# Kernel tuning notes

Measured on AMD Instinct MI355X. Metric: run time of the kernel, lower is better.

## Reference

```python
import jax, jax.numpy as jnp
import numpy as np

N, M, D = 4096, 8192, 512

def setup_inputs() -> dict:
    key = jax.random.key(0)
    k1, k2, k3, k4 = jax.random.split(key, 4)
    X = jax.random.normal(k1, (N, D), dtype=jnp.float32)
    SV = jax.random.normal(k2, (M, D), dtype=jnp.float32)
    DC = jax.random.normal(k3, (1, M), dtype=jnp.float32)
    IC = jax.random.normal(k4, (1,), dtype=jnp.float32)
    gamma = jnp.float32(1.0 / D)
    return {"X": X, "SV": SV, "DC": DC, "IC": IC, "gamma": gamma}

def reference(X, SV, DC, IC, gamma):
    # Squared pairwise L2 distances via GEMM expansion (same math as
    # ||SV - x||^2 without materializing the [N, M, D] broadcast tensor):
    # d2[n, m] = ||x_n||^2 + ||sv_m||^2 - 2 * x_n . sv_m
    x2 = jnp.sum(X * X, axis=1)          # [N]
    sv2 = jnp.sum(SV * SV, axis=1)       # [M]
    cross = jnp.einsum("nd,md->nm", X, SV)  # [N, M]
    d2 = jnp.maximum(x2[:, None] + sv2[None, :] - 2.0 * cross, 0.0)
    k = jnp.exp(-gamma * d2)             # RBF kernel values [N, M]
    # Weighted reduction over support vectors + intercept -> decision values [N]
    return jnp.sum(k * DC, axis=1) + IC
```

## Files before the change

### kernel.cpp

```cpp
#include <hip/hip_runtime.h>
#include <stdint.h>

#define NN 4096
#define MM 8192
#define DD 512
#define KT 8

typedef __bf16 bf16x8 __attribute__((ext_vector_type(8)));
typedef __bf16 bf16x4 __attribute__((ext_vector_type(4)));
typedef float f32x4 __attribute__((ext_vector_type(4)));
typedef float f32x16 __attribute__((ext_vector_type(16)));

__device__ __forceinline__ void load_lds16(const void* g, void* l) {
  __builtin_amdgcn_global_load_lds(
      (const __attribute__((address_space(1))) unsigned int*)g,
      (__attribute__((address_space(3))) unsigned int*)l, 16, 0, 0);
}

__global__ __launch_bounds__(256) void convert_norm_kernel(
    const float* __restrict__ X, const float* __restrict__ SV,
    __bf16* __restrict__ Xb, __bf16* __restrict__ SVb,
    float* __restrict__ x2, float* __restrict__ sv2,
    float* __restrict__ out, const float* __restrict__ IC) {
  int wid = blockIdx.x * 4 + (threadIdx.x >> 6);
  int lane = threadIdx.x & 63;
  const float* src;
  __bf16* dst;
  float* nrm;
  if (wid < NN) {
    src = X + (size_t)wid * DD;
    dst = Xb + (size_t)wid * DD;
    nrm = x2 + wid;
    if (lane == 0) out[wid] = IC[0];
  } else {
    int r = wid - NN;
    src = SV + (size_t)r * DD;
    dst = SVb + (size_t)r * DD;
    nrm = sv2 + r;
  }
  const f32x4* s = (const f32x4*)src;
  f32x4 a = s[lane];
  f32x4 b = s[lane + 64];
  float sum = a.x * a.x + a.y * a.y + a.z * a.z + a.w * a.w +
              b.x * b.x + b.y * b.y + b.z * b.z + b.w * b.w;
  bf16x4 ca = {(__bf16)a.x, (__bf16)a.y, (__bf16)a.z, (__bf16)a.w};
  bf16x4 cb = {(__bf16)b.x, (__bf16)b.y, (__bf16)b.z, (__bf16)b.w};
  *(bf16x4*)(dst + 4 * lane) = ca;
  *(bf16x4*)(dst + 256 + 4 * lane) = cb;
#pragma unroll
  for (int m = 32; m >= 1; m >>= 1) sum += __shfl_xor(sum, m, 64);
  if (lane == 0) *nrm = sum;
}

__global__ __launch_bounds__(384, 3) void rbf_gemm_kernel(
    const bf16x8* __restrict__ Xb, const bf16x8* __restrict__ SVb,
    const float* __restrict__ x2, const float* __restrict__ sv2,
    const float* __restrict__ DC, const float* __restrict__ gamma_p,
    float* __restrict__ out) {
  __shared__ bf16x8 As[2][1024];
  __shared__ bf16x8 Bs[2][1024];

  const int t = threadIdx.x;
  const int lane = t & 63;
  const int wave = t >> 6;
  const int n0 = blockIdx.x * 128;
  const int m0 = blockIdx.y * 128;

  const int wave_m = wave & 1;
  const int wave_n = wave >> 1;
  const int l31 = lane & 31;
  const int lhi = lane >> 5;

  const int rg = lane >> 3;
  const int perm = (lane & 7) ^ rg;

  f32x16 acc[2][2];
#pragma unroll
  for (int i = 0; i < 2; ++i)
#pragma unroll
    for (int j = 0; j < 2; ++j)
#pragma unroll
      for (int r = 0; r < 16; ++r) acc[i][j][r] = 0.0f;

  if (wave == 4) {
#pragma unroll
    for (int it = 0; it < 16; ++it)
      load_lds16(Xb + (size_t)(n0 + it * 8 + rg) * 64 + perm, &As[0][it * 64 + lane]);
  } else if (wave == 5) {
#pragma unroll
    for (int it = 0; it < 16; ++it)
      load_lds16(SVb + (size_t)(m0 + it * 8 + rg) * 64 + perm, &Bs[0][it * 64 + lane]);
  }
  __syncthreads();

#pragma unroll
  for (int kt = 0; kt < KT; ++kt) {
    const int cur = kt & 1;
    const int nxt = cur ^ 1;
    if (wave == 4) {
      if (kt + 1 < KT) {
#pragma unroll
        for (int it = 0; it < 16; ++it)
          load_lds16(Xb + (size_t)(n0 + it * 8 + rg) * 64 + (kt + 1) * 8 + perm,
                     &As[nxt][it * 64 + lane]);
      }
    } else if (wave == 5) {
      if (kt + 1 < KT) {
#pragma unroll
        for (int it = 0; it < 16; ++it)
          load_lds16(SVb + (size_t)(m0 + it * 8 + rg) * 64 + (kt + 1) * 8 + perm,
                     &Bs[nxt][it * 64 + lane]);
      }
    } else {
#pragma unroll
      for (int ks = 0; ks < 4; ++ks) {
        const int kc = ks * 2 + lhi;
        const int sw = kc ^ (l31 & 7);
        const int ra = (wave_n * 64 + l31) * 8;
        const int rb = (wave_m * 64 + l31) * 8;
        bf16x8 af0 = As[cur][ra + sw];
        bf16x8 af1 = As[cur][ra + 256 + sw];
        bf16x8 bf0 = Bs[cur][rb + sw];
        bf16x8 bf1 = Bs[cur][rb + 256 + sw];
        acc[0][0] = __builtin_amdgcn_mfma_f32_32x32x16_bf16(af0, bf0, acc[0][0], 0, 0, 0);
        acc[0][1] = __builtin_amdgcn_mfma_f32_32x32x16_bf16(af0, bf1, acc[0][1], 0, 0, 0);
        acc[1][0] = __builtin_amdgcn_mfma_f32_32x32x16_bf16(af1, bf0, acc[1][0], 0, 0, 0);
        acc[1][1] = __builtin_amdgcn_mfma_f32_32x32x16_bf16(af1, bf1, acc[1][1], 0, 0, 0);
      }
    }
    __syncthreads();
  }

  if (wave < 4) {
    const float g = gamma_p[0];
    const float c2 = g * 1.4426950408889634f;

    float sv2v[2], dcv[2];
    const int colb = m0 + wave_m * 64 + l31;
    sv2v[0] = sv2[colb];
    dcv[0] = DC[colb];
    sv2v[1] = sv2[colb + 32];
    dcv[1] = DC[colb + 32];

#pragma unroll
    for (int i = 0; i < 2; ++i) {
      const int rowb = n0 + wave_n * 64 + i * 32 + 4 * lhi;
      float val[16];
#pragma unroll
      for (int g4 = 0; g4 < 4; ++g4) {
        f32x4 xv = *(const f32x4*)(x2 + rowb + 8 * g4);
#pragma unroll
        for (int r2 = 0; r2 < 4; ++r2) {
          const int reg = g4 * 4 + r2;
          float v = 0.0f;
#pragma unroll
          for (int j = 0; j < 2; ++j) {
            float d2 = xv[r2] + sv2v[j] - 2.0f * acc[i][j][reg];
            d2 = fmaxf(d2, 0.0f);
            v += exp2f(-c2 * d2) * dcv[j];
          }
          val[reg] = v;
        }
      }
#pragma unroll
      for (int m = 1; m < 32; m <<= 1)
#pragma unroll
        for (int reg = 0; reg < 16; ++reg)
          val[reg] += __shfl_xor(val[reg], m, 64);
      if (l31 == 0) {
#pragma unroll
        for (int g4 = 0; g4 < 4; ++g4)
#pragma unroll
          for (int r2 = 0; r2 < 4; ++r2)
            atomicAdd(&out[rowb + 8 * g4 + r2], val[g4 * 4 + r2]);
      }
    }
  }
}

extern "C" void kernel_launch(void* const* d_in, const int* in_sizes, int n_in,
                              void* d_out, int out_size, void* d_ws, size_t ws_size,
                              hipStream_t stream) {
  const float* X = (const float*)d_in[0];
  const float* SV = (const float*)d_in[1];
  const float* DC = (const float*)d_in[2];
  const float* IC = (const float*)d_in[3];
  const float* gamma = (const float*)d_in[4];
  float* out = (float*)d_out;

  char* ws = (char*)d_ws;
  __bf16* Xb = (__bf16*)ws;
  __bf16* SVb = (__bf16*)(ws + (size_t)NN * DD * 2);
  float* x2 = (float*)(ws + (size_t)(NN + MM) * DD * 2);
  float* sv2 = x2 + NN;

  convert_norm_kernel<<<(NN + MM) / 4, 256, 0, stream>>>(X, SV, Xb, SVb, x2, sv2, out, IC);
  dim3 grid(NN / 128, MM / 128);
  rbf_gemm_kernel<<<grid, 384, 0, stream>>>((const bf16x8*)Xb, (const bf16x8*)SVb,
                                            x2, sv2, DC, gamma, out);
}
```

Baseline: 151.2 us.

## Replace producer-wave double buffering with single-buffer cooperative loads

Drops the two dedicated loader waves and the double-buffered LDS. All four compute waves now cooperatively load each K tile into a single buffer, synchronize, then run the MFMAs. This halves LDS use and removes the idle producer waves, so more blocks can fit per CU (launch bounds raised to 4). The cost is that global-to-LDS loads are no longer overlapped with compute inside a block, and the design relies on other resident blocks to hide that latency.

After: 136.7 us. 9.6% less time.

```diff
diff --git a/kernel.cpp b/kernel.cpp
--- a/kernel.cpp
+++ b/kernel.cpp
@@ -52,13 +52,13 @@
   if (lane == 0) *nrm = sum;
 }
 
-__global__ __launch_bounds__(384, 3) void rbf_gemm_kernel(
+__global__ __launch_bounds__(256, 4) void rbf_gemm_kernel(
     const bf16x8* __restrict__ Xb, const bf16x8* __restrict__ SVb,
     const float* __restrict__ x2, const float* __restrict__ sv2,
     const float* __restrict__ DC, const float* __restrict__ gamma_p,
     float* __restrict__ out) {
-  __shared__ bf16x8 As[2][1024];
-  __shared__ bf16x8 Bs[2][1024];
+  __shared__ bf16x8 As[1024];
+  __shared__ bf16x8 Bs[1024];
 
   const int t = threadIdx.x;
   const int lane = t & 63;
@@ -71,8 +71,8 @@
   const int l31 = lane & 31;
   const int lhi = lane >> 5;
 
-  const int rg = lane >> 3;
-  const int perm = (lane & 7) ^ rg;
+  const int srow = t >> 3;
+  const int sslot = t & 7;
 
   f32x16 acc[2][2];
 #pragma unroll
@@ -82,98 +82,75 @@
 #pragma unroll
       for (int r = 0; r < 16; ++r) acc[i][j][r] = 0.0f;
 
-  if (wave == 4) {
+  for (int kt = 0; kt < KT; ++kt) {
 #pragma unroll
-    for (int it = 0; it < 16; ++it)
-      load_lds16(Xb + (size_t)(n0 + it * 8 + rg) * 64 + perm, &As[0][it * 64 + lane]);
-  } else if (wave == 5) {
+    for (int it = 0; it < 4; ++it) {
+      const int c = it * 256 + t;
+      const int row = it * 32 + srow;
+      const int kg = sslot ^ (row & 7);
+      load_lds16(Xb + (size_t)(n0 + row) * 64 + kt * 8 + kg, &As[c]);
+      load_lds16(SVb + (size_t)(m0 + row) * 64 + kt * 8 + kg, &Bs[c]);
+    }
+    __syncthreads();
 #pragma unroll
-    for (int it = 0; it < 16; ++it)
-      load_lds16(SVb + (size_t)(m0 + it * 8 + rg) * 64 + perm, &Bs[0][it * 64 + lane]);
-  }
-  __syncthreads();
-
-#pragma unroll
-  for (int kt = 0; kt < KT; ++kt) {
-    const int cur = kt & 1;
-    const int nxt = cur ^ 1;
-    if (wave == 4) {
-      if (kt + 1 < KT) {
-#pragma unroll
-        for (int it = 0; it < 16; ++it)
-          load_lds16(Xb + (size_t)(n0 + it * 8 + rg) * 64 + (kt + 1) * 8 + perm,
-                     &As[nxt][it * 64 + lane]);
-      }
-    } else if (wave == 5) {
-      if (kt + 1 < KT) {
-#pragma unroll
-        for (int it = 0; it < 16; ++it)
-          load_lds16(SVb + (size_t)(m0 + it * 8 + rg) * 64 + (kt + 1) * 8 + perm,
-                     &Bs[nxt][it * 64 + lane]);
-      }
-    } else {
-#pragma unroll
-      for (int ks = 0; ks < 4; ++ks) {
-        const int kc = ks * 2 + lhi;
-        const int sw = kc ^ (l31 & 7);
-        const int ra = (wave_n * 64 + l31) * 8;
-        const int rb = (wave_m * 64 + l31) * 8;
-        bf16x8 af0 = As[cur][ra + sw];
-        bf16x8 af1 = As[cur][ra + 256 + sw];
-        bf16x8 bf0 = Bs[cur][rb + sw];
-        bf16x8 bf1 = Bs[cur][rb + 256 + sw];
-        acc[0][0] = __builtin_amdgcn_mfma_f32_32x32x16_bf16(af0, bf0, acc[0][0], 0, 0, 0);
-        acc[0][1] = __builtin_amdgcn_mfma_f32_32x32x16_bf16(af0, bf1, acc[0][1], 0, 0, 0);
-        acc[1][0] = __builtin_amdgcn_mfma_f32_32x32x16_bf16(af1, bf0, acc[1][0], 0, 0, 0);
-        acc[1][1] = __builtin_amdgcn_mfma_f32_32x32x16_bf16(af1, bf1, acc[1][1], 0, 0, 0);
-      }
+    for (int ks = 0; ks < 4; ++ks) {
+      const int kc = ks * 2 + lhi;
+      const int sw = kc ^ (l31 & 7);
+      const int ra = (wave_n * 64 + l31) * 8;
+      const int rb = (wave_m * 64 + l31) * 8;
+      bf16x8 af0 = As[ra + sw];
+      bf16x8 af1 = As[ra + 256 + sw];
+      bf16x8 bf0 = Bs[rb + sw];
+      bf16x8 bf1 = Bs[rb + 256 + sw];
+      acc[0][0] = __builtin_amdgcn_mfma_f32_32x32x16_bf16(af0, bf0, acc[0][0], 0, 0, 0);
+      acc[0][1] = __builtin_amdgcn_mfma_f32_32x32x16_bf16(af0, bf1, acc[0][1], 0, 0, 0);
+      acc[1][0] = __builtin_amdgcn_mfma_f32_32x32x16_bf16(af1, bf0, acc[1][0], 0, 0, 0);
+      acc[1][1] = __builtin_amdgcn_mfma_f32_32x32x16_bf16(af1, bf1, acc[1][1], 0, 0, 0);
     }
     __syncthreads();
   }
 
-  if (wave < 4) {
-    const float g = gamma_p[0];
-    const float c2 = g * 1.4426950408889634f;
+  const float g = gamma_p[0];
+  const float c2 = g * 1.4426950408889634f;
 
-    float sv2v[2], dcv[2];
-    const int colb = m0 + wave_m * 64 + l31;
-    sv2v[0] = sv2[colb];
-    dcv[0] = DC[colb];
-    sv2v[1] = sv2[colb + 32];
-    dcv[1] = DC[colb + 32];
+  float sv2v[2], dcv[2];
+  const int colb = m0 + wave_m * 64 + l31;
+  sv2v[0] = sv2[colb];
+  dcv[0] = DC[colb];
+  sv2v[1] = sv2[colb + 32];
+  dcv[1] = DC[colb + 32];
 
 #pragma unroll
-    for (int i = 0; i < 2; ++i) {
-      const int rowb = n0 + wave_n * 64 + i * 32 + 4 * lhi;
-      float val[16];
+  for (int i = 0; i < 2; ++i) {
+    const int rowb = n0 + wave_n * 64 + i * 32 + 4 * lhi;
+    float val[16];
 #pragma unroll
-      for (int g4 = 0; g4 < 4; ++g4) {
-        f32x4 xv = *(const f32x4*)(x2 + rowb + 8 * g4);
+    for (int g4 = 0; g4 < 4; ++g4) {
+      f32x4 xv = *(const f32x4*)(x2 + rowb + 8 * g4);
 #pragma unroll
-        for (int r2 = 0; r2 < 4; ++r2) {
-          const int reg = g4 * 4 + r2;
-          float v = 0.0f;
+      for (int r2 = 0; r2 < 4; ++r2) {
+        const int reg = g4 * 4 + r2;
+        float v = 0.0f;
 #pragma unroll
-          for (int j = 0; j < 2; ++j) {
-            float d2 = xv[r2] + sv2v[j] - 2.0f * acc[i][j][reg];
-            d2 = fmaxf(d2, 0.0f);
-            v += exp2f(-c2 * d2) * dcv[j];
-          }
-          val[reg] = v;
+        for (int j = 0; j < 2; ++j) {
+          float d2 = xv[r2] + sv2v[j] - 2.0f * acc[i][j][reg];
+          d2 = fmaxf(d2, 0.0f);
+          v += exp2f(-c2 * d2) * dcv[j];
         }
+        val[reg] = v;
       }
+    }
 #pragma unroll
-      for (int m = 1; m < 32; m <<= 1)
+    for (int m = 1; m < 32; m <<= 1)
 #pragma unroll
-        for (int reg = 0; reg < 16; ++reg)
-          val[reg] += __shfl_xor(val[reg], m, 64);
-      if (l31 == 0) {
+      for (int reg = 0; reg < 16; ++reg)
+        val[reg] += __shfl_xor(val[reg], m, 64);
+    if (l31 == 0) {
 #pragma unroll
-        for (int g4 = 0; g4 < 4; ++g4)
+      for (int g4 = 0; g4 < 4; ++g4)
 #pragma unroll
-          for (int r2 = 0; r2 < 4; ++r2)
-            atomicAdd(&out[rowb + 8 * g4 + r2], val[g4 * 4 + r2]);
-      }
+        for (int r2 = 0; r2 < 4; ++r2)
+          atomicAdd(&out[rowb + 8 * g4 + r2], val[g4 * 4 + r2]);
     }
   }
 }
@@ -196,6 +173,6 @@
 
   convert_norm_kernel<<<(NN + MM) / 4, 256, 0, stream>>>(X, SV, Xb, SVb, x2, sv2, out, IC);
   dim3 grid(NN / 128, MM / 128);
-  rbf_gemm_kernel<<<grid, 384, 0, stream>>>((const bf16x8*)Xb, (const bf16x8*)SVb,
+  rbf_gemm_kernel<<<grid, 256, 0, stream>>>((const bf16x8*)Xb, (const bf16x8*)SVb,
                                             x2, sv2, DC, gamma, out);
 }
```
